# Performance work log

Hardware: AMD Instinct MI355X
Metric: run time of the kernel (lower is better)

## Reference

```python
import jax, jax.numpy as jnp
import numpy as np
import math

HEADS = 8

def setup_inputs() -> dict:
    key = jax.random.key(0)
    k1, k2 = jax.random.split(key)
    B, C, H, W = 8, 512, 32, 32
    x = jax.random.normal(k1, (B, C, H, W), dtype=jnp.float32)
    # weight-norm 1x1 conv params: v ~ N(0, 0.05), g initialized to ||v|| (torch weight_norm default)
    proj_v = jax.random.normal(k2, (3 * C, C), dtype=jnp.float32) * 0.05
    proj_g = jnp.linalg.norm(proj_v, axis=1)
    proj_b = jnp.zeros((3 * C,), dtype=jnp.float32)
    return {"x": x, "proj_v": proj_v, "proj_g": proj_g, "proj_b": proj_b}

def reference(x, proj_v, proj_g, proj_b):
    B, C, H, W = x.shape
    heads = HEADS
    dim = C // heads
    N = H * W
    # weight-normalized 1x1 conv: w = g * v / ||v|| per output channel
    w = proj_g[:, None] * proj_v / jnp.linalg.norm(proj_v, axis=1, keepdims=True)
    c = jnp.einsum('oc,bchw->bohw', w, x) + proj_b[None, :, None, None]
    c = c.reshape(B, 3, heads, dim, N)
    q, k, v = c[:, 0], c[:, 1], c[:, 2]  # each (B, heads, dim, N)
    scale = 1.0 / math.sqrt(dim)
    attn = jnp.einsum('bhdq,bhdk->bhqk', q, k) * scale  # (B, heads, N, N)
    attn = jax.nn.softmax(attn, axis=-1)
    out = jnp.einsum('bhdk,bhqk->bhdq', v, attn)  # (B, heads, dim, N)
    return x + out.reshape(B, C, H, W)
```

## Files before the change

### kernel.cpp

```cpp
#include <hip/hip_runtime.h>

typedef _Float16 f16;
typedef _Float16 f16x2 __attribute__((ext_vector_type(2)));
typedef _Float16 f16x4 __attribute__((ext_vector_type(4)));
typedef _Float16 f16x8 __attribute__((ext_vector_type(8)));
typedef float f32x4 __attribute__((ext_vector_type(4)));
typedef unsigned int u32;

__device__ inline f32x4 mfma16(f16x8 a, f16x8 b, f32x4 c) {
    return __builtin_amdgcn_mfma_f32_16x16x32_f16(a, b, c, 0, 0, 0);
}

__device__ inline f16x2 pk2(float a, float b) {
    return __builtin_bit_cast(f16x2, __builtin_amdgcn_cvt_pkrtz(a, b));
}

__device__ inline void st8(f16* p, f16x8 v) {
    *(f16x4*)p = __builtin_shufflevector(v, v, 0, 1, 2, 3);
    *(f16x4*)(p + 4) = __builtin_shufflevector(v, v, 4, 5, 6, 7);
}
__device__ inline f16x8 ld8(const f16* p) {
    f16x4 lo = *(const f16x4*)p;
    f16x4 hi = *(const f16x4*)(p + 4);
    return __builtin_shufflevector(lo, hi, 0, 1, 2, 3, 4, 5, 6, 7);
}

__device__ inline void gl2lds16(const f16* g, f16* l) {
    __builtin_amdgcn_global_load_lds(
        (const __attribute__((address_space(1))) u32*)g,
        (__attribute__((address_space(3))) u32*)l, 16, 0, 0);
}

__global__ __launch_bounds__(256) void compute_w_k(const float* __restrict__ pv,
                                                   const float* __restrict__ pg,
                                                   f16* __restrict__ w) {
    int o = blockIdx.x;
    const float* row = pv + (size_t)o * 512;
    float s = 0.f;
    for (int c = threadIdx.x; c < 512; c += 256) { float t = row[c]; s += t * t; }
    for (int off = 32; off; off >>= 1) s += __shfl_down(s, off, 64);
    __shared__ float red[4];
    int lane = threadIdx.x & 63, wid = threadIdx.x >> 6;
    if (lane == 0) red[wid] = s;
    __syncthreads();
    float tot = red[0] + red[1] + red[2] + red[3];
    float scale = pg[o] * rsqrtf(tot);
    for (int c = threadIdx.x; c < 512; c += 256)
        w[(size_t)o * 512 + c] = (f16)(row[c] * scale);
}

__global__ __launch_bounds__(256) void transpose_x_k(const float* __restrict__ x,
                                                     f16* __restrict__ xT) {
    __shared__ float t[32][33];
    int b = blockIdx.z, n0 = blockIdx.x * 32, c0 = blockIdx.y * 32;
    int tx = threadIdx.x, ty = threadIdx.y;
    const float* xb = x + (size_t)b * 512 * 1024;
    for (int i = 0; i < 4; i++)
        t[ty + 8 * i][tx] = xb[(size_t)(c0 + ty + 8 * i) * 1024 + n0 + tx];
    __syncthreads();
    f16* xTb = xT + (size_t)b * 1024 * 512;
    for (int i = 0; i < 4; i++)
        xTb[(size_t)(n0 + ty + 8 * i) * 512 + c0 + tx] = (f16)t[tx][ty + 8 * i];
}

__global__ __launch_bounds__(256) void qkv_gemm_k(const f16* __restrict__ w,
                                                  const f16* __restrict__ xT,
                                                  const float* __restrict__ pb,
                                                  f16* __restrict__ qk,
                                                  f16* __restrict__ v) {
    __shared__ f16 lA[128 * 64];
    __shared__ f16 lB[128 * 64];
    int b = blockIdx.z;
    int oBase = blockIdx.y * 128;
    int nBase = blockIdx.x * 128;
    const f16* xb = xT + (size_t)b * 1024 * 512;
    int tid = threadIdx.x, lane = tid & 63, warp = tid >> 6;
    int wy = warp >> 1, wx = warp & 1;
    int quad = lane >> 4, l15 = lane & 15;

    int srow = lane >> 3;
    int schunk = (lane & 7) ^ srow;
    const f16* aSrc[4]; const f16* bSrc[4]; f16* aDst[4]; f16* bDst[4];
    for (int j = 0; j < 4; j++) {
        int rb = (warp * 4 + j) * 8;
        aSrc[j] = w  + (size_t)(oBase + rb + srow) * 512 + schunk * 8;
        bSrc[j] = xb + (size_t)(nBase + rb + srow) * 512 + schunk * 8;
        aDst[j] = lA + rb * 64;
        bDst[j] = lB + rb * 64;
    }
    int ph0 = (quad ^ (l15 & 7)) * 8;
    int ph1 = ((4 + quad) ^ (l15 & 7)) * 8;

    f32x4 acc[4][4] = {};

    for (int k0 = 0; k0 < 512; k0 += 64) {
        __syncthreads();
        for (int j = 0; j < 4; j++) {
            gl2lds16(aSrc[j] + k0, aDst[j]);
            gl2lds16(bSrc[j] + k0, bDst[j]);
        }
        __syncthreads();
        for (int kh = 0; kh < 2; kh++) {
            int ph = kh ? ph1 : ph0;
            f16x8 af[4], bf[4];
            for (int mi = 0; mi < 4; mi++)
                af[mi] = *(f16x8*)&lA[(wy * 64 + mi * 16 + l15) * 64 + ph];
            for (int ni = 0; ni < 4; ni++)
                bf[ni] = *(f16x8*)&lB[(wx * 64 + ni * 16 + l15) * 64 + ph];
            for (int mi = 0; mi < 4; mi++)
                for (int ni = 0; ni < 4; ni++)
                    acc[mi][ni] = mfma16(af[mi], bf[ni], acc[mi][ni]);
        }
    }

    for (int mi = 0; mi < 4; mi++) {
        int oRow = oBase + wy * 64 + mi * 16 + quad * 4;
        for (int ni = 0; ni < 4; ni++) {
            int n = nBase + wx * 64 + ni * 16 + l15;
            for (int reg = 0; reg < 4; reg++) {
                int oo = oRow + reg;
                float val = acc[mi][ni][reg] + pb[oo];
                int sel = oo >> 9, h = (oo >> 6) & 7, d = oo & 63;
                if (sel == 0) val *= 0.125f;
                if (sel < 2)
                    qk[((((size_t)b * 2 + sel) * 8 + h) * 1024 + n) * 64 + d] = (f16)val;
                else
                    v[(((size_t)b * 8 + h) * 64 + d) * 1024 + n] = (f16)val;
            }
        }
    }
}

#define ALDK 68
__global__ __launch_bounds__(256) void attn_k(const f16* __restrict__ qk,
                                              const f16* __restrict__ vg,
                                              const float* __restrict__ x,
                                              float* __restrict__ out) {
    __shared__ __align__(16) f16 smem[3 * 64 * ALDK];
    f16* lK = smem;
    f16* lV = smem + 64 * ALDK;
    f16* lPb = smem + 2 * 64 * ALDK;
    float* OT = (float*)smem;

    int bh = blockIdx.y;
    int b = bh >> 3, h = bh & 7;
    int qBase = blockIdx.x * 64;
    int tid = threadIdx.x, lane = tid & 63, warp = tid >> 6;
    int quad = lane >> 4, l15 = lane & 15;

    const f16* qbase = qk + (((size_t)b * 2 + 0) * 8 + h) * 1024 * 64;
    const f16* kbase = qk + (((size_t)b * 2 + 1) * 8 + h) * 1024 * 64;
    const f16* vbase = vg + ((size_t)b * 8 + h) * 64 * 1024;
    f16* lP = lPb + warp * 16 * ALDK;

    int q0 = qBase + warp * 16;
    f16x8 aq[2];
    for (int kh = 0; kh < 2; kh++)
        aq[kh] = *(const f16x8*)&qbase[(size_t)(q0 + l15) * 64 + kh * 32 + quad * 8];

    int sr0 = tid >> 3, sc0 = (tid & 7) * 8;
    int sr1 = (tid + 256) >> 3, sc1 = sc0;

    f16x8 rK[2], rV[2];
    rK[0] = *(const f16x8*)&kbase[(size_t)sr0 * 64 + sc0];
    rK[1] = *(const f16x8*)&kbase[(size_t)sr1 * 64 + sc1];
    rV[0] = *(const f16x8*)&vbase[(size_t)sr0 * 1024 + sc0];
    rV[1] = *(const f16x8*)&vbase[(size_t)sr1 * 1024 + sc1];

    f32x4 accO[4] = {};
    float l_cur = 0.f;

    for (int kt = 0; kt < 16; kt++) {
        __syncthreads();
        st8(&lK[sr0 * ALDK + sc0], rK[0]);
        st8(&lK[sr1 * ALDK + sc1], rK[1]);
        st8(&lV[sr0 * ALDK + sc0], rV[0]);
        st8(&lV[sr1 * ALDK + sc1], rV[1]);
        __syncthreads();
        if (kt < 15) {
            const f16* kb = kbase + (size_t)(kt + 1) * 64 * 64;
            rK[0] = *(const f16x8*)&kb[(size_t)sr0 * 64 + sc0];
            rK[1] = *(const f16x8*)&kb[(size_t)sr1 * 64 + sc1];
            rV[0] = *(const f16x8*)&vbase[(size_t)sr0 * 1024 + (kt + 1) * 64 + sc0];
            rV[1] = *(const f16x8*)&vbase[(size_t)sr1 * 1024 + (kt + 1) * 64 + sc1];
        }

        f32x4 st[4] = {};
        for (int mt = 0; mt < 4; mt++)
            for (int kh = 0; kh < 2; kh++) {
                f16x8 ak = ld8(&lK[(mt * 16 + l15) * ALDK + kh * 32 + quad * 8]);
                st[mt] = mfma16(ak, aq[kh], st[mt]);
            }

        float rs0 = 0.f, rs1 = 0.f, rs2 = 0.f, rs3 = 0.f;
        for (int mt = 0; mt < 4; mt++) {
            float p0 = __expf(st[mt][0]);
            float p1 = __expf(st[mt][1]);
            float p2 = __expf(st[mt][2]);
            float p3 = __expf(st[mt][3]);
            rs0 += p0; rs1 += p1; rs2 += p2; rs3 += p3;
            f16x2 lo = pk2(p0, p1);
            f16x2 hi = pk2(p2, p3);
            f16x4 pk;
            pk[0] = lo[0]; pk[1] = lo[1]; pk[2] = hi[0]; pk[3] = hi[1];
            *(f16x4*)&lP[l15 * ALDK + mt * 16 + quad * 4] = pk;
        }
        float rs = (rs0 + rs1) + (rs2 + rs3);
        rs += __shfl_xor(rs, 16, 64);
        rs += __shfl_xor(rs, 32, 64);
        l_cur += rs;

        for (int kh = 0; kh < 2; kh++) {
            f16x8 bp = ld8(&lP[l15 * ALDK + kh * 32 + quad * 8]);
            for (int dt = 0; dt < 4; dt++) {
                f16x8 av = ld8(&lV[(dt * 16 + l15) * ALDK + kh * 32 + quad * 8]);
                accO[dt] = mfma16(av, bp, accO[dt]);
            }
        }
    }

    __syncthreads();
    float rl = 1.0f / l_cur;
    for (int dt = 0; dt < 4; dt++)
        for (int r = 0; r < 4; r++)
            OT[(dt * 16 + quad * 4 + r) * ALDK + warp * 16 + l15] = accO[dt][r] * rl;
    __syncthreads();
    for (int i = 0; i < 4; i++) {
        int cid = tid + 256 * i;
        int d = cid >> 4, qi = (cid & 15) * 4;
        float4 o4 = *(float4*)&OT[d * ALDK + qi];
        size_t gi = ((size_t)b * 512 + h * 64 + d) * 1024 + qBase + qi;
        float4 xv = *(const float4*)&x[gi];
        o4.x += xv.x; o4.y += xv.y; o4.z += xv.z; o4.w += xv.w;
        *(float4*)&out[gi] = o4;
    }
}

extern "C" void kernel_launch(void* const* d_in, const int* in_sizes, int n_in,
                              void* d_out, int out_size, void* d_ws, size_t ws_size,
                              hipStream_t stream) {
    (void)in_sizes; (void)n_in; (void)out_size; (void)ws_size;
    const float* x  = (const float*)d_in[0];
    const float* pv = (const float*)d_in[1];
    const float* pg = (const float*)d_in[2];
    const float* pb = (const float*)d_in[3];
    float* out = (float*)d_out;

    char* ws = (char*)d_ws;
    f16* w   = (f16*)(ws);
    f16* xT  = (f16*)(ws + 1572864);
    f16* qk  = (f16*)(ws + 1572864 + 8388608);
    f16* v   = (f16*)(ws + 1572864 + 8388608 + 16777216);

    hipLaunchKernelGGL(compute_w_k,  dim3(1536),      dim3(256),   0, stream, pv, pg, w);
    hipLaunchKernelGGL(transpose_x_k, dim3(32, 16, 8), dim3(32, 8), 0, stream, x, xT);
    hipLaunchKernelGGL(qkv_gemm_k,   dim3(8, 12, 8),  dim3(256),   0, stream, w, xT, pb, qk, v);
    hipLaunchKernelGGL(attn_k,       dim3(16, 64),    dim3(256),   0, stream, qk, v, x, out);
}
```

Measured before the change: 154.5 us.

## Double-buffer LDS tiles in QKV GEMM and vectorize Q/K epilogue stores

The QKV projection GEMM now uses two LDS buffers per operand, so the global-to-LDS copy of the next K-slice is issued before computing on the current slice, and one of the two barriers per iteration is dropped. The epilogue hoists the q/k/v selector to block level and writes Q/K outputs as packed 4-element f16 stores instead of scalar stores. This doubles shared memory use in the GEMM kernel, which may lower occupancy. The single barrier relies on the async LDS copies having completed before the next iteration reads them.

After: 142.9 us. -7.5%, faster.

```diff
diff --git a/kernel.cpp b/kernel.cpp
--- a/kernel.cpp
+++ b/kernel.cpp
@@ -68,8 +68,8 @@
                                                   const float* __restrict__ pb,
                                                   f16* __restrict__ qk,
                                                   f16* __restrict__ v) {
-    __shared__ f16 lA[128 * 64];
-    __shared__ f16 lB[128 * 64];
+    __shared__ f16 lA[2][128 * 64];
+    __shared__ f16 lB[2][128 * 64];
     int b = blockIdx.z;
     int oBase = blockIdx.y * 128;
     int nBase = blockIdx.x * 128;
@@ -80,52 +80,66 @@
 
     int srow = lane >> 3;
     int schunk = (lane & 7) ^ srow;
-    const f16* aSrc[4]; const f16* bSrc[4]; f16* aDst[4]; f16* bDst[4];
+    const f16* aS[4]; const f16* bS[4]; int dOff[4];
     for (int j = 0; j < 4; j++) {
         int rb = (warp * 4 + j) * 8;
-        aSrc[j] = w  + (size_t)(oBase + rb + srow) * 512 + schunk * 8;
-        bSrc[j] = xb + (size_t)(nBase + rb + srow) * 512 + schunk * 8;
-        aDst[j] = lA + rb * 64;
-        bDst[j] = lB + rb * 64;
+        aS[j] = w  + (size_t)(oBase + rb + srow) * 512 + schunk * 8;
+        bS[j] = xb + (size_t)(nBase + rb + srow) * 512 + schunk * 8;
+        dOff[j] = rb * 64;
     }
     int ph0 = (quad ^ (l15 & 7)) * 8;
     int ph1 = ((4 + quad) ^ (l15 & 7)) * 8;
 
+    for (int j = 0; j < 4; j++) {
+        gl2lds16(aS[j], &lA[0][dOff[j]]);
+        gl2lds16(bS[j], &lB[0][dOff[j]]);
+    }
+
     f32x4 acc[4][4] = {};
 
-    for (int k0 = 0; k0 < 512; k0 += 64) {
+    for (int i = 0; i < 8; i++) {
         __syncthreads();
-        for (int j = 0; j < 4; j++) {
-            gl2lds16(aSrc[j] + k0, aDst[j]);
-            gl2lds16(bSrc[j] + k0, bDst[j]);
-        }
-        __syncthreads();
+        if (i < 7) {
+            int k0 = (i + 1) * 64, bb = (i + 1) & 1;
+            for (int j = 0; j < 4; j++) {
+                gl2lds16(aS[j] + k0, &lA[bb][dOff[j]]);
+                gl2lds16(bS[j] + k0, &lB[bb][dOff[j]]);
+            }
+        }
+        const f16* cA = lA[i & 1];
+        const f16* cB = lB[i & 1];
         for (int kh = 0; kh < 2; kh++) {
             int ph = kh ? ph1 : ph0;
             f16x8 af[4], bf[4];
             for (int mi = 0; mi < 4; mi++)
-                af[mi] = *(f16x8*)&lA[(wy * 64 + mi * 16 + l15) * 64 + ph];
+                af[mi] = *(f16x8*)&cA[(wy * 64 + mi * 16 + l15) * 64 + ph];
             for (int ni = 0; ni < 4; ni++)
-                bf[ni] = *(f16x8*)&lB[(wx * 64 + ni * 16 + l15) * 64 + ph];
+                bf[ni] = *(f16x8*)&cB[(wx * 64 + ni * 16 + l15) * 64 + ph];
             for (int mi = 0; mi < 4; mi++)
                 for (int ni = 0; ni < 4; ni++)
                     acc[mi][ni] = mfma16(af[mi], bf[ni], acc[mi][ni]);
         }
     }
 
+    int selB = oBase >> 9;
     for (int mi = 0; mi < 4; mi++) {
         int oRow = oBase + wy * 64 + mi * 16 + quad * 4;
+        int h = (oRow >> 6) & 7, d0 = oRow & 63;
         for (int ni = 0; ni < 4; ni++) {
             int n = nBase + wx * 64 + ni * 16 + l15;
-            for (int reg = 0; reg < 4; reg++) {
-                int oo = oRow + reg;
-                float val = acc[mi][ni][reg] + pb[oo];
-                int sel = oo >> 9, h = (oo >> 6) & 7, d = oo & 63;
-                if (sel == 0) val *= 0.125f;
-                if (sel < 2)
-                    qk[((((size_t)b * 2 + sel) * 8 + h) * 1024 + n) * 64 + d] = (f16)val;
-                else
-                    v[(((size_t)b * 8 + h) * 64 + d) * 1024 + n] = (f16)val;
+            if (selB < 2) {
+                float sc = selB == 0 ? 0.125f : 1.0f;
+                f16x4 o4;
+                o4[0] = (f16)((acc[mi][ni][0] + pb[oRow + 0]) * sc);
+                o4[1] = (f16)((acc[mi][ni][1] + pb[oRow + 1]) * sc);
+                o4[2] = (f16)((acc[mi][ni][2] + pb[oRow + 2]) * sc);
+                o4[3] = (f16)((acc[mi][ni][3] + pb[oRow + 3]) * sc);
+                *(f16x4*)&qk[((((size_t)b * 2 + selB) * 8 + h) * 1024 + n) * 64 + d0] = o4;
+            } else {
+                for (int reg = 0; reg < 4; reg++) {
+                    float val = acc[mi][ni][reg] + pb[oRow + reg];
+                    v[(((size_t)b * 8 + h) * 64 + d0 + reg) * 1024 + n] = (f16)val;
+                }
             }
         }
     }
```
